# Kernel tuning notes

Hardware: AMD Instinct MI355X
Metric: run time of the kernel (lower is better)

The kernel has to match this reference:

```python
import jax, jax.numpy as jnp
import numpy as np

D = 768      # qkv.in_features (ViT-Base)
R = 16       # LoRA rank
T = 8        # task_id: number of previously saved adapters
B_, S_ = 32, 256
TAU = 1.0


def setup_inputs() -> dict:
    key = jax.random.key(0)
    ks = jax.random.split(key, 13)
    s = lambda k, shape, sc=0.02: jax.random.normal(k, shape, jnp.float32) * sc
    return {
        "x": jax.random.normal(ks[0], (B_, S_, D), jnp.float32),
        "qkv_w": s(ks[1], (3 * D, D)),           # torch Linear weight [out,in]
        "qkv_b": s(ks[2], (3 * D,)),
        "la_q": s(ks[3], (R, D)),                # current-task LoRA A_q [r,d]
        "lb_q": s(ks[4], (D, R)),                # current-task LoRA B_q [d,r]
        "la_v": s(ks[5], (R, D)),
        "lb_v": s(ks[6], (D, R)),
        "A_q": s(ks[7], (T, R, D)),              # saved per-task A_q stacks
        "B_q": s(ks[8], (T, D, R)),
        "A_v": s(ks[9], (T, R, D)),
        "B_v": s(ks[10], (T, D, R)),
        "gate_logits": jax.random.normal(ks[11], (T,), jnp.float32),
        "alpha": jnp.ones((T + 1,), jnp.float32),  # gumbel_gate.alpha, indexed by task_id
    }


def _moe_branch(x, A, B, beta):
    """Weighted sum over T tasks of (x @ A_t^T @ B_t^T) / (||A_t||*||B_t||), weight beta_t.

    Vectorizes the per-task serial low-rank matmuls of the torch loop into two
    batched einsums; beta/norm scaling is folded into B to avoid materializing
    per-task [B,S,D] outputs.
    """
    nA = jnp.sqrt(jnp.sum(A * A, axis=(1, 2)))   # [T] Frobenius norms
    nB = jnp.sqrt(jnp.sum(B * B, axis=(1, 2)))
    scale = beta / (nA * nB)                      # [T]
    za = jnp.einsum('bsd,trd->bstr', x, A)       # [B,S,T,r]
    Bs = B * scale[:, None, None]                 # [T,D,r]
    return jnp.einsum('bstr,tdr->bsd', za, Bs)   # [B,S,D]


def _lora(x, a, b):
    # torch: b(a(x)) with Linear weights a:[r,d], b:[d,r]
    return jnp.einsum('bsr,dr->bsd', jnp.einsum('bsd,rd->bsr', x, a), b)


def reference(x, qkv_w, qkv_b, la_q, lb_q, la_v, lb_v, A_q, B_q, A_v, B_v, gate_logits, alpha):
    # Gumbel-softmax gate over tasks (deterministic/eval path: softmax(logits/tau), hard=False)
    beta = jax.nn.softmax(gate_logits / TAU)
    a_cur = alpha[T]  # alpha[self.task_id]
    new_q = _moe_branch(x, A_q, B_q, beta) + a_cur * _lora(x, la_q, lb_q)
    new_v = _moe_branch(x, A_v, B_v, beta) + a_cur * _lora(x, la_v, lb_v)
    qkv = jnp.einsum('bsd,ed->bse', x, qkv_w) + qkv_b  # [B,S,3D]
    qkv = qkv.at[..., :D].add(new_q)
    qkv = qkv.at[..., 2 * D:].add(new_v)
    return qkv
```

## Files before the change

### kernel.cpp

```cpp
#include <hip/hip_runtime.h>

#define TOK 8192
#define DD  768
#define NOUT 2304
#define TT  8
#define RR  16
#define KRANK 144

typedef __bf16 bf16;
typedef __bf16 bf16x4 __attribute__((ext_vector_type(4)));
typedef __bf16 bf16x8 __attribute__((ext_vector_type(8)));
typedef float  floatx4 __attribute__((ext_vector_type(4)));

__device__ __forceinline__ void gl_lds16(const void* g, void* l) {
    __builtin_amdgcn_global_load_lds((const __attribute__((address_space(1))) void*)g,
                                     (__attribute__((address_space(3))) void*)l, 16, 0, 0);
}

__global__ __launch_bounds__(256) void prep_kernel(
    const float* __restrict__ A_q, const float* __restrict__ B_q,
    const float* __restrict__ A_v, const float* __restrict__ B_v,
    const float* __restrict__ x, bf16* __restrict__ xb,
    float* __restrict__ norms)
{
    __shared__ float ws4[4];
    const int b = blockIdx.x;
    if (b < 32) {
        const float* base;
        switch (b >> 3) {
            case 0: base = A_q; break;
            case 1: base = B_q; break;
            case 2: base = A_v; break;
            default: base = B_v; break;
        }
        base += (b & 7) * (RR * DD);
        float s = 0.f;
        for (int i = threadIdx.x; i < RR * DD; i += 256) {
            float v = base[i];
            s = fmaf(v, v, s);
        }
        #pragma unroll
        for (int off = 32; off > 0; off >>= 1) s += __shfl_down(s, off);
        if ((threadIdx.x & 63) == 0) ws4[threadIdx.x >> 6] = s;
        __syncthreads();
        if (threadIdx.x == 0)
            norms[b] = sqrtf(ws4[0] + ws4[1] + ws4[2] + ws4[3]);
    } else {
        const int idx = ((b - 32) * 256 + threadIdx.x) * 8;
        const float4 v0 = *(const float4*)(x + idx);
        const float4 v1 = *(const float4*)(x + idx + 4);
        bf16x8 o = { (bf16)v0.x, (bf16)v0.y, (bf16)v0.z, (bf16)v0.w,
                     (bf16)v1.x, (bf16)v1.y, (bf16)v1.z, (bf16)v1.w };
        *(bf16x8*)(xb + idx) = o;
    }
}

__global__ __launch_bounds__(256) void fold_kernel(
    const float* __restrict__ qkv_w,
    const float* __restrict__ A_q, const float* __restrict__ la_q,
    const float* __restrict__ B_q, const float* __restrict__ lb_q,
    const float* __restrict__ A_v, const float* __restrict__ la_v,
    const float* __restrict__ B_v, const float* __restrict__ lb_v,
    const float* __restrict__ gate_logits, const float* __restrict__ alpha,
    const float* __restrict__ norms, bf16* __restrict__ Wc)
{
    const int tid = threadIdx.x;
    const int d = blockIdx.x * 256 + tid;
    const int gy = blockIdx.y;

    if (gy >= 96 && gy < 192) {
        const int rowbase = DD + (gy - 96) * 8;
        #pragma unroll
        for (int j = 0; j < 8; ++j) {
            const int row = rowbase + j;
            Wc[row * DD + d] = (bf16)qkv_w[row * DD + d];
        }
        return;
    }

    __shared__ float c_lds[8 * KRANK];
    __shared__ float sc_sh[TT];
    __shared__ float acur_sh;

    const bool is_v = (gy >= 192);
    const int e0 = (is_v ? gy - 192 : gy) * 8;
    const float* Astack = is_v ? A_v : A_q;
    const float* la     = is_v ? la_v : la_q;
    const float* Bmat   = is_v ? B_v : B_q;
    const float* lb     = is_v ? lb_v : lb_q;
    const float* nA     = norms + (is_v ? 16 : 0);
    const float* nB     = norms + (is_v ? 24 : 8);
    const int rowbase   = (is_v ? 2 * DD : 0) + e0;

    if (tid == 0) {
        float mx = gate_logits[0];
        for (int t = 1; t < TT; ++t) mx = fmaxf(mx, gate_logits[t]);
        float e[TT], s = 0.f;
        for (int t = 0; t < TT; ++t) { e[t] = __expf(gate_logits[t] - mx); s += e[t]; }
        for (int t = 0; t < TT; ++t) sc_sh[t] = (e[t] / s) / (nA[t] * nB[t]);
        acur_sh = alpha[TT];
    }
    __syncthreads();

    for (int idx = tid; idx < 8 * KRANK; idx += 256) {
        const int j = idx / KRANK, i = idx - j * KRANK;
        const int e = e0 + j;
        float v;
        if (i < TT * RR) {
            const int t = i >> 4, r = i & 15;
            v = sc_sh[t] * Bmat[(t * DD + e) * RR + r];
        } else {
            v = acur_sh * lb[e * RR + (i - TT * RR)];
        }
        c_lds[j * KRANK + i] = v;
    }
    __syncthreads();

    float acc[8] = {0.f, 0.f, 0.f, 0.f, 0.f, 0.f, 0.f, 0.f};

    for (int i = 0; i < TT * RR; i += 4) {
        const float a0 = Astack[(i + 0) * DD + d];
        const float a1 = Astack[(i + 1) * DD + d];
        const float a2 = Astack[(i + 2) * DD + d];
        const float a3 = Astack[(i + 3) * DD + d];
        #pragma unroll
        for (int j = 0; j < 8; ++j) {
            const float4 cv = *(const float4*)&c_lds[j * KRANK + i];
            acc[j] = fmaf(a0, cv.x, fmaf(a1, cv.y, fmaf(a2, cv.z, fmaf(a3, cv.w, acc[j]))));
        }
    }
    #pragma unroll
    for (int i = 0; i < RR; i += 4) {
        const float a0 = la[(i + 0) * DD + d];
        const float a1 = la[(i + 1) * DD + d];
        const float a2 = la[(i + 2) * DD + d];
        const float a3 = la[(i + 3) * DD + d];
        #pragma unroll
        for (int j = 0; j < 8; ++j) {
            const float4 cv = *(const float4*)&c_lds[j * KRANK + TT * RR + i];
            acc[j] = fmaf(a0, cv.x, fmaf(a1, cv.y, fmaf(a2, cv.z, fmaf(a3, cv.w, acc[j]))));
        }
    }

    #pragma unroll
    for (int j = 0; j < 8; ++j) {
        const int row = rowbase + j;
        Wc[row * DD + d] = (bf16)(qkv_w[row * DD + d] + acc[j]);
    }
}

__global__ __launch_bounds__(256, 3) void gemm_kernel(
    const bf16* __restrict__ A, const bf16* __restrict__ B,
    const float* __restrict__ bias, float* __restrict__ C)
{
    __shared__ __align__(16) char smem[40960];
    bf16* const lds_a = (bf16*)smem;
    bf16* const lds_b = (bf16*)(smem + 16384);

    const int tid  = threadIdx.x;
    const int lane = tid & 63;
    const int wave = tid >> 6;

    const int flat  = blockIdx.x;
    const int xcd   = flat & 7;
    const int local = flat >> 3;
    const int mb    = xcd * 8 + (local & 7);
    const int nb    = local >> 3;
    const int m0 = mb * 128;
    const int n0 = nb * 192;

    const int wm = (wave >> 1) * 64;
    const int wn = (wave & 1) * 96;

    const int srow = lane >> 3;
    const int scol = ((lane & 7) ^ srow) * 8;

    floatx4 acc[4][6];
    #pragma unroll
    for (int i = 0; i < 4; ++i)
        #pragma unroll
        for (int j = 0; j < 6; ++j)
            acc[i][j] = (floatx4){0.f, 0.f, 0.f, 0.f};

    const bf16* const gA = A + (m0 + srow) * DD + scol;
    const bf16* const gB = B + (n0 + srow) * DD + scol;

    for (int kt = 0; kt < DD / 64; ++kt) {
        const int k0 = kt * 64;
        #pragma unroll
        for (int i = 0; i < 4; ++i) {
            const int j = i * 4 + wave;
            gl_lds16(gA + j * 8 * DD + k0, &lds_a[j * 512]);
        }
        #pragma unroll
        for (int i = 0; i < 6; ++i) {
            const int j = i * 4 + wave;
            gl_lds16(gB + j * 8 * DD + k0, &lds_b[j * 512]);
        }
        __syncthreads();

        #pragma unroll
        for (int ks = 0; ks < 2; ++ks) {
            const int c_log = ks * 4 + (lane >> 4);
            bf16x8 af[4];
            #pragma unroll
            for (int mt = 0; mt < 4; ++mt) {
                const int r = wm + mt * 16 + (lane & 15);
                af[mt] = *(const bf16x8*)&lds_a[r * 64 + ((c_log ^ (r & 7)) * 8)];
            }
            #pragma unroll
            for (int nt = 0; nt < 6; ++nt) {
                const int r = wn + nt * 16 + (lane & 15);
                const bf16x8 bfr = *(const bf16x8*)&lds_b[r * 64 + ((c_log ^ (r & 7)) * 8)];
                #pragma unroll
                for (int mt = 0; mt < 4; ++mt)
                    acc[mt][nt] = __builtin_amdgcn_mfma_f32_16x16x32_bf16(
                        af[mt], bfr, acc[mt][nt], 0, 0, 0);
            }
        }
        __syncthreads();
    }

    const int cr = (lane >> 4) * 4;
    const int cc = lane & 15;
    #pragma unroll
    for (int nt = 0; nt < 6; ++nt) {
        const int gn = n0 + wn + nt * 16 + cc;
        const float bv = bias[gn];
        #pragma unroll
        for (int mt = 0; mt < 4; ++mt) {
            const int gmb = m0 + wm + mt * 16 + cr;
            #pragma unroll
            for (int r = 0; r < 4; ++r)
                C[(gmb + r) * NOUT + gn] = acc[mt][nt][r] + bv;
        }
    }
}

extern "C" void kernel_launch(void* const* d_in, const int* in_sizes, int n_in,
                              void* d_out, int out_size, void* d_ws, size_t ws_size,
                              hipStream_t stream)
{
    const float* x           = (const float*)d_in[0];
    const float* qkv_w       = (const float*)d_in[1];
    const float* qkv_b       = (const float*)d_in[2];
    const float* la_q        = (const float*)d_in[3];
    const float* lb_q        = (const float*)d_in[4];
    const float* la_v        = (const float*)d_in[5];
    const float* lb_v        = (const float*)d_in[6];
    const float* A_q         = (const float*)d_in[7];
    const float* B_q         = (const float*)d_in[8];
    const float* A_v         = (const float*)d_in[9];
    const float* B_v         = (const float*)d_in[10];
    const float* gate_logits = (const float*)d_in[11];
    const float* alpha       = (const float*)d_in[12];
    float* out = (float*)d_out;

    char* ws = (char*)d_ws;
    bf16*  Xbf    = (bf16*)ws;
    bf16*  Wc     = (bf16*)(ws + 12582912);
    float* norms  = (float*)(ws + 12582912 + 3538944);

    prep_kernel<<<32 + TOK * DD / 2048, 256, 0, stream>>>(A_q, B_q, A_v, B_v,
                                                          x, Xbf, norms);
    fold_kernel<<<dim3(3, 288), 256, 0, stream>>>(qkv_w,
                                                  A_q, la_q, B_q, lb_q,
                                                  A_v, la_v, B_v, lb_v,
                                                  gate_logits, alpha, norms, Wc);
    gemm_kernel<<<768, 256, 0, stream>>>(Xbf, Wc, qkv_b, out);
}
```

Measured before the change: 172.0 us.

## Widen GEMM tile to 128x288 with 6 waves and 32x32x16 MFMA

Reworks the bf16 GEMM so each block computes a 128x288 output tile with 384 threads (6 waves, each 64x96) using 32x32x16 MFMA instructions instead of 16x16x32. The grid shrinks from 768 to 512 blocks and the K-tile loads are spread across all six waves. The final redundant barrier is skipped. The wider tile and larger MFMA shape are meant to raise operand reuse per LDS read and per global load, at the cost of more LDS per block and possible occupancy or register-pressure changes.

```diff
diff --git a/kernel.cpp b/kernel.cpp
--- a/kernel.cpp
+++ b/kernel.cpp
@@ -11,6 +11,7 @@
 typedef __bf16 bf16x4 __attribute__((ext_vector_type(4)));
 typedef __bf16 bf16x8 __attribute__((ext_vector_type(8)));
 typedef float  floatx4 __attribute__((ext_vector_type(4)));
+typedef float  floatx16 __attribute__((ext_vector_type(16)));
 
 __device__ __forceinline__ void gl_lds16(const void* g, void* l) {
     __builtin_amdgcn_global_load_lds((const __attribute__((address_space(1))) void*)g,
@@ -149,11 +150,11 @@
     }
 }
 
-__global__ __launch_bounds__(256, 3) void gemm_kernel(
+__global__ __launch_bounds__(384, 3) void gemm_kernel(
     const bf16* __restrict__ A, const bf16* __restrict__ B,
     const float* __restrict__ bias, float* __restrict__ C)
 {
-    __shared__ __align__(16) char smem[40960];
+    __shared__ __align__(16) char smem[53248];
     bf16* const lds_a = (bf16*)smem;
     bf16* const lds_b = (bf16*)(smem + 16384);
 
@@ -167,72 +168,72 @@
     const int mb    = xcd * 8 + (local & 7);
     const int nb    = local >> 3;
     const int m0 = mb * 128;
-    const int n0 = nb * 192;
-
-    const int wm = (wave >> 1) * 64;
-    const int wn = (wave & 1) * 96;
+    const int n0 = nb * 288;
+
+    const int wm = (wave & 1) * 64;
+    const int wn = (wave >> 1) * 96;
 
     const int srow = lane >> 3;
     const int scol = ((lane & 7) ^ srow) * 8;
 
-    floatx4 acc[4][6];
-    #pragma unroll
-    for (int i = 0; i < 4; ++i)
-        #pragma unroll
-        for (int j = 0; j < 6; ++j)
-            acc[i][j] = (floatx4){0.f, 0.f, 0.f, 0.f};
+    floatx16 acc[2][3];
+    #pragma unroll
+    for (int i = 0; i < 2; ++i)
+        #pragma unroll
+        for (int j = 0; j < 3; ++j)
+            acc[i][j] = (floatx16)(0.f);
 
     const bf16* const gA = A + (m0 + srow) * DD + scol;
     const bf16* const gB = B + (n0 + srow) * DD + scol;
 
+    const int l31 = lane & 31;
+    const int kg  = lane >> 5;
+    const int aoff0 = (wm +  0 + l31) * 64;
+    const int aoff1 = (wm + 32 + l31) * 64;
+    const int boff0 = (wn +  0 + l31) * 64;
+    const int boff1 = (wn + 32 + l31) * 64;
+    const int boff2 = (wn + 64 + l31) * 64;
+
     for (int kt = 0; kt < DD / 64; ++kt) {
         const int k0 = kt * 64;
-        #pragma unroll
-        for (int i = 0; i < 4; ++i) {
-            const int j = i * 4 + wave;
-            gl_lds16(gA + j * 8 * DD + k0, &lds_a[j * 512]);
-        }
-        #pragma unroll
-        for (int i = 0; i < 6; ++i) {
-            const int j = i * 4 + wave;
-            gl_lds16(gB + j * 8 * DD + k0, &lds_b[j * 512]);
+        for (int c = wave; c < 52; c += 6) {
+            if (c < 16) gl_lds16(gA + c * 8 * DD + k0, lds_a + c * 512);
+            else        gl_lds16(gB + (c - 16) * 8 * DD + k0, lds_b + (c - 16) * 512);
         }
         __syncthreads();
 
         #pragma unroll
-        for (int ks = 0; ks < 2; ++ks) {
-            const int c_log = ks * 4 + (lane >> 4);
-            bf16x8 af[4];
+        for (int ks = 0; ks < 4; ++ks) {
+            const int sw = (((ks << 1) | kg) ^ (lane & 7)) << 3;
+            const bf16x8 af0 = *(const bf16x8*)&lds_a[aoff0 + sw];
+            const bf16x8 af1 = *(const bf16x8*)&lds_a[aoff1 + sw];
+            const bf16x8 bf0 = *(const bf16x8*)&lds_b[boff0 + sw];
+            const bf16x8 bf1 = *(const bf16x8*)&lds_b[boff1 + sw];
+            const bf16x8 bf2 = *(const bf16x8*)&lds_b[boff2 + sw];
+            acc[0][0] = __builtin_amdgcn_mfma_f32_32x32x16_bf16(af0, bf0, acc[0][0], 0, 0, 0);
+            acc[1][0] = __builtin_amdgcn_mfma_f32_32x32x16_bf16(af1, bf0, acc[1][0], 0, 0, 0);
+            acc[0][1] = __builtin_amdgcn_mfma_f32_32x32x16_bf16(af0, bf1, acc[0][1], 0, 0, 0);
+            acc[1][1] = __builtin_amdgcn_mfma_f32_32x32x16_bf16(af1, bf1, acc[1][1], 0, 0, 0);
+            acc[0][2] = __builtin_amdgcn_mfma_f32_32x32x16_bf16(af0, bf2, acc[0][2], 0, 0, 0);
+            acc[1][2] = __builtin_amdgcn_mfma_f32_32x32x16_bf16(af1, bf2, acc[1][2], 0, 0, 0);
+        }
+        if (kt != DD / 64 - 1) __syncthreads();
+    }
+
+    const int cn = lane & 31;
+    const int rb = (lane >> 5) * 4;
+    #pragma unroll
+    for (int nt = 0; nt < 3; ++nt) {
+        const int gn = n0 + wn + nt * 32 + cn;
+        const float bv = bias[gn];
+        #pragma unroll
+        for (int mt = 0; mt < 2; ++mt) {
+            const int gm = m0 + wm + mt * 32 + rb;
             #pragma unroll
-            for (int mt = 0; mt < 4; ++mt) {
-                const int r = wm + mt * 16 + (lane & 15);
-                af[mt] = *(const bf16x8*)&lds_a[r * 64 + ((c_log ^ (r & 7)) * 8)];
+            for (int reg = 0; reg < 16; ++reg) {
+                const int row = gm + (reg & 3) + 8 * (reg >> 2);
+                C[row * NOUT + gn] = acc[mt][nt][reg] + bv;
             }
-            #pragma unroll
-            for (int nt = 0; nt < 6; ++nt) {
-                const int r = wn + nt * 16 + (lane & 15);
-                const bf16x8 bfr = *(const bf16x8*)&lds_b[r * 64 + ((c_log ^ (r & 7)) * 8)];
-                #pragma unroll
-                for (int mt = 0; mt < 4; ++mt)
-                    acc[mt][nt] = __builtin_amdgcn_mfma_f32_16x16x32_bf16(
-                        af[mt], bfr, acc[mt][nt], 0, 0, 0);
-            }
-        }
-        __syncthreads();
-    }
-
-    const int cr = (lane >> 4) * 4;
-    const int cc = lane & 15;
-    #pragma unroll
-    for (int nt = 0; nt < 6; ++nt) {
-        const int gn = n0 + wn + nt * 16 + cc;
-        const float bv = bias[gn];
-        #pragma unroll
-        for (int mt = 0; mt < 4; ++mt) {
-            const int gmb = m0 + wm + mt * 16 + cr;
-            #pragma unroll
-            for (int r = 0; r < 4; ++r)
-                C[(gmb + r) * NOUT + gn] = acc[mt][nt][r] + bv;
         }
     }
 }
@@ -267,5 +268,5 @@
                                                   A_q, la_q, B_q, lb_q,
                                                   A_v, la_v, B_v, lb_v,
                                                   gate_logits, alpha, norms, Wc);
-    gemm_kernel<<<768, 256, 0, stream>>>(Xbf, Wc, qkv_b, out);
-}
+    gemm_kernel<<<512, 384, 0, stream>>>(Xbf, Wc, qkv_b, out);
+}
```

Result: slower. 196.9 us (+14.4%).

## Fuse fp32-to-bf16 conversion of x into the GEMM A-tile load

Applied to the files above, without the earlier changes.

Drops the separate pass that converts x to bf16 in the prep kernel. The GEMM now loads fp32 x directly into registers, converts it, and writes bf16 into swizzled LDS. This removes a 25 MB read plus 12.5 MB write round trip through the workspace. In exchange, each GEMM block reads fp32 A twice as wide, and every N-block (12 of them) re-reads x, through synchronous register loads instead of async global-to-LDS. It also skips the trailing barrier on the last k-iteration.

```diff
diff --git a/kernel.cpp b/kernel.cpp
--- a/kernel.cpp
+++ b/kernel.cpp
@@ -20,39 +20,29 @@
 __global__ __launch_bounds__(256) void prep_kernel(
     const float* __restrict__ A_q, const float* __restrict__ B_q,
     const float* __restrict__ A_v, const float* __restrict__ B_v,
-    const float* __restrict__ x, bf16* __restrict__ xb,
     float* __restrict__ norms)
 {
     __shared__ float ws4[4];
     const int b = blockIdx.x;
-    if (b < 32) {
-        const float* base;
-        switch (b >> 3) {
-            case 0: base = A_q; break;
-            case 1: base = B_q; break;
-            case 2: base = A_v; break;
-            default: base = B_v; break;
-        }
-        base += (b & 7) * (RR * DD);
-        float s = 0.f;
-        for (int i = threadIdx.x; i < RR * DD; i += 256) {
-            float v = base[i];
-            s = fmaf(v, v, s);
-        }
-        #pragma unroll
-        for (int off = 32; off > 0; off >>= 1) s += __shfl_down(s, off);
-        if ((threadIdx.x & 63) == 0) ws4[threadIdx.x >> 6] = s;
-        __syncthreads();
-        if (threadIdx.x == 0)
-            norms[b] = sqrtf(ws4[0] + ws4[1] + ws4[2] + ws4[3]);
-    } else {
-        const int idx = ((b - 32) * 256 + threadIdx.x) * 8;
-        const float4 v0 = *(const float4*)(x + idx);
-        const float4 v1 = *(const float4*)(x + idx + 4);
-        bf16x8 o = { (bf16)v0.x, (bf16)v0.y, (bf16)v0.z, (bf16)v0.w,
-                     (bf16)v1.x, (bf16)v1.y, (bf16)v1.z, (bf16)v1.w };
-        *(bf16x8*)(xb + idx) = o;
-    }
+    const float* base;
+    switch (b >> 3) {
+        case 0: base = A_q; break;
+        case 1: base = B_q; break;
+        case 2: base = A_v; break;
+        default: base = B_v; break;
+    }
+    base += (b & 7) * (RR * DD);
+    float s = 0.f;
+    for (int i = threadIdx.x; i < RR * DD; i += 256) {
+        float v = base[i];
+        s = fmaf(v, v, s);
+    }
+    #pragma unroll
+    for (int off = 32; off > 0; off >>= 1) s += __shfl_down(s, off);
+    if ((threadIdx.x & 63) == 0) ws4[threadIdx.x >> 6] = s;
+    __syncthreads();
+    if (threadIdx.x == 0)
+        norms[b] = sqrtf(ws4[0] + ws4[1] + ws4[2] + ws4[3]);
 }
 
 __global__ __launch_bounds__(256) void fold_kernel(
@@ -150,7 +140,7 @@
 }
 
 __global__ __launch_bounds__(256, 3) void gemm_kernel(
-    const bf16* __restrict__ A, const bf16* __restrict__ B,
+    const float* __restrict__ X, const bf16* __restrict__ B,
     const float* __restrict__ bias, float* __restrict__ C)
 {
     __shared__ __align__(16) char smem[40960];
@@ -182,20 +172,31 @@
         for (int j = 0; j < 6; ++j)
             acc[i][j] = (floatx4){0.f, 0.f, 0.f, 0.f};
 
-    const bf16* const gA = A + (m0 + srow) * DD + scol;
-    const bf16* const gB = B + (n0 + srow) * DD + scol;
+    const float* const gAf = X + (m0 + srow) * DD + scol;
+    const bf16*  const gB  = B + (n0 + srow) * DD + scol;
 
     for (int kt = 0; kt < DD / 64; ++kt) {
         const int k0 = kt * 64;
+
+        float4 av0[4], av1[4];
         #pragma unroll
         for (int i = 0; i < 4; ++i) {
-            const int j = i * 4 + wave;
-            gl_lds16(gA + j * 8 * DD + k0, &lds_a[j * 512]);
+            const int c = i * 4 + wave;
+            const float* p = gAf + c * 8 * DD + k0;
+            av0[i] = *(const float4*)p;
+            av1[i] = *(const float4*)(p + 4);
         }
         #pragma unroll
         for (int i = 0; i < 6; ++i) {
             const int j = i * 4 + wave;
             gl_lds16(gB + j * 8 * DD + k0, &lds_b[j * 512]);
+        }
+        #pragma unroll
+        for (int i = 0; i < 4; ++i) {
+            const int c = i * 4 + wave;
+            bf16x8 o = { (bf16)av0[i].x, (bf16)av0[i].y, (bf16)av0[i].z, (bf16)av0[i].w,
+                         (bf16)av1[i].x, (bf16)av1[i].y, (bf16)av1[i].z, (bf16)av1[i].w };
+            *(bf16x8*)&lds_a[c * 512 + lane * 8] = o;
         }
         __syncthreads();
 
@@ -218,7 +219,7 @@
                         af[mt], bfr, acc[mt][nt], 0, 0, 0);
             }
         }
-        __syncthreads();
+        if (kt != DD / 64 - 1) __syncthreads();
     }
 
     const int cr = (lane >> 4) * 4;
@@ -257,15 +258,13 @@
     float* out = (float*)d_out;
 
     char* ws = (char*)d_ws;
-    bf16*  Xbf    = (bf16*)ws;
-    bf16*  Wc     = (bf16*)(ws + 12582912);
-    float* norms  = (float*)(ws + 12582912 + 3538944);
-
-    prep_kernel<<<32 + TOK * DD / 2048, 256, 0, stream>>>(A_q, B_q, A_v, B_v,
-                                                          x, Xbf, norms);
+    bf16*  Wc     = (bf16*)ws;
+    float* norms  = (float*)(ws + 3538944);
+
+    prep_kernel<<<32, 256, 0, stream>>>(A_q, B_q, A_v, B_v, norms);
     fold_kernel<<<dim3(3, 288), 256, 0, stream>>>(qkv_w,
                                                   A_q, la_q, B_q, lb_q,
                                                   A_v, la_v, B_v, lb_v,
                                                   gate_logits, alpha, norms, Wc);
-    gemm_kernel<<<768, 256, 0, stream>>>(Xbf, Wc, qkv_b, out);
-}
+    gemm_kernel<<<768, 256, 0, stream>>>(x, Wc, qkv_b, out);
+}
```

After: 180.1 us. +4.7%, slower.
